# Kernel optimization log

Hardware: AMD Instinct MI355X
Metric: run time of the kernel (lower is better)

Reference implementation:

```python
import jax, jax.numpy as jnp
import numpy as np

N = 1 << 20          # number of segment duration values
NUM_EDGES = 100      # quantile bin edges (arange(0,1,0.01))
VOCAB = 101          # embedding rows
DIM = 128


def setup_inputs() -> dict:
    key = jax.random.key(0)
    k1, k2, k3 = jax.random.split(key, 3)
    # duration values in [0, 60) seconds
    time_value = jax.random.uniform(k1, (N,), dtype=jnp.float32) * 60.0
    # quantile edges of the duration distribution: sorted by construction
    bin_edges = jnp.sort(jax.random.uniform(k2, (NUM_EDGES,), dtype=jnp.float32) * 60.0)
    embed_table = jax.random.normal(k3, (VOCAB, DIM), dtype=jnp.float32)
    return {"time_value": time_value, "bin_edges": bin_edges, "embed_table": embed_table}


def reference(time_value, bin_edges, embed_table):
    # Fused, batched version of the original per-element loop:
    # torch.searchsorted(edges, dv) -> bucket index in [0, NUM_EDGES]
    idx = jnp.searchsorted(bin_edges, time_value, side="left")  # [N] int32
    # embedding lookup -> [N, DIM]
    return jnp.take(embed_table, idx, axis=0)
```

## Files before the change

kernel.cpp:

```cpp
#include <hip/hip_runtime.h>


#define MAX_EDGES 128
#define PAD_INF 3.402823466e+38f

__global__ __launch_bounds__(256) void compute_idx_kernel(
    const float* __restrict__ time_value,
    const float* __restrict__ bin_edges,
    int* __restrict__ idx,
    unsigned int n, int num_edges)
{
    __shared__ float s_edges[MAX_EDGES];
    if (threadIdx.x < MAX_EDGES)
        s_edges[threadIdx.x] = (threadIdx.x < (unsigned)num_edges)
                                   ? bin_edges[threadIdx.x] : PAD_INF;
    __syncthreads();

    const unsigned int stride = gridDim.x * blockDim.x;
    for (unsigned int i = blockIdx.x * blockDim.x + threadIdx.x;
         i < n; i += stride) {
        float v = time_value[i];
        int lo = 0;
        #pragma unroll
        for (int step = 64; step > 0; step >>= 1)
            lo += (s_edges[lo + step - 1] < v) ? step : 0;
        idx[i] = lo;
    }
}

__global__ __launch_bounds__(256) void gather_f4_32(
    const int* __restrict__ idx,
    const float* __restrict__ embed_table,
    float* __restrict__ out,
    unsigned int n)
{
    const float4* t4 = (const float4*)embed_table;
    float4* o4 = (float4*)out;

    const unsigned int total  = n << 3;
    const unsigned int stride = gridDim.x * blockDim.x;

    for (unsigned int j = blockIdx.x * blockDim.x + threadIdx.x;
         j < total; j += stride) {
        unsigned int row = j >> 3;
        unsigned int o   = j & 7u;
        unsigned int lo  = (unsigned int)idx[row];
        unsigned int tb  = (lo  << 5) + o;
        unsigned int ob  = (row << 5) + o;
        float4 a = t4[tb];
        float4 b = t4[tb + 8];
        float4 c = t4[tb + 16];
        float4 d = t4[tb + 24];
        o4[ob]      = a;
        o4[ob + 8]  = b;
        o4[ob + 16] = c;
        o4[ob + 24] = d;
    }
}

__device__ __forceinline__ int lower_bound_lds(const float* s_edges, int num_edges, float v) {
    int lo = 0, hi = num_edges;
    while (lo < hi) {
        int mid = (lo + hi) >> 1;
        if (s_edges[mid] < v) lo = mid + 1; else hi = mid;
    }
    return lo;
}

__global__ __launch_bounds__(256) void duration_encoding_generic(
    const float* __restrict__ time_value,
    const float* __restrict__ bin_edges,
    const float* __restrict__ embed_table,
    float* __restrict__ out,
    unsigned int n, int num_edges, unsigned int f4_per_row)
{
    __shared__ float s_edges[MAX_EDGES];
    for (int i = threadIdx.x; i < num_edges; i += blockDim.x)
        s_edges[i] = bin_edges[i];
    __syncthreads();

    const unsigned long long total  = (unsigned long long)n * f4_per_row;
    const unsigned long long stride = (unsigned long long)gridDim.x * blockDim.x;
    const float4* table4 = (const float4*)embed_table;
    float4* out4 = (float4*)out;

    for (unsigned long long j = (unsigned long long)blockIdx.x * blockDim.x + threadIdx.x;
         j < total; j += stride) {
        unsigned int row = (unsigned int)(j / f4_per_row);
        unsigned int c4  = (unsigned int)(j - (unsigned long long)row * f4_per_row);
        float v = time_value[row];
        int lo = lower_bound_lds(s_edges, num_edges, v);
        out4[j] = table4[(unsigned long long)lo * f4_per_row + c4];
    }
}

extern "C" void kernel_launch(void* const* d_in, const int* in_sizes, int n_in,
                              void* d_out, int out_size, void* d_ws, size_t ws_size,
                              hipStream_t stream) {
    const float* time_value  = (const float*)d_in[0];
    const float* bin_edges   = (const float*)d_in[1];
    const float* embed_table = (const float*)d_in[2];
    float* out = (float*)d_out;

    const unsigned int n         = (unsigned int)in_sizes[0];
    const int          num_edges = in_sizes[1];
    const unsigned int dim       = (unsigned int)(out_size / in_sizes[0]);
    const unsigned int f4_per_row = dim / 4;

    const int block = 256;

    if (f4_per_row == 32u && num_edges <= MAX_EDGES && ws_size >= (size_t)n * 4) {
        int* idx = (int*)d_ws;

        unsigned int b1 = (n + block - 1) / block;
        int grid1 = (int)(b1 < 4096u ? b1 : 4096u);
        compute_idx_kernel<<<grid1, block, 0, stream>>>(
            time_value, bin_edges, idx, n, num_edges);

        const unsigned int total = n << 3;
        unsigned int b2 = (total + block - 1) / block;
        int grid2 = (int)(b2 < 2048u ? b2 : 2048u);
        gather_f4_32<<<grid2, block, 0, stream>>>(idx, embed_table, out, n);
    } else {
        const unsigned long long total = (unsigned long long)n * f4_per_row;
        unsigned long long bn = (total + block - 1) / block;
        int grid = (int)(bn < 2048ull ? bn : 2048ull);
        duration_encoding_generic<<<grid, block, 0, stream>>>(
            time_value, bin_edges, embed_table, out, n, num_edges, f4_per_row);
    }
}
```

Measured before the change: 119.5 us.

## Vectorize index search and use one-shot strided gather without grid-stride loops

The index kernel now reads four time values per thread as a float4 and writes four indices as an int4, launching one thread per group of four with no grid-stride loop. The gather kernel drops its grid-stride loop and launches one thread per n*8 float4 slot. Each thread handles four float4s spaced T apart in the flattened output, so every store instruction across a wavefront is fully contiguous. The aim is to cut loop overhead and improve memory-level parallelism with larger grids. The trade-off is many more blocks and an extra idx load per float4.

After: 109.9 us. 8.0% less time.

```diff
diff --git a/kernel.cpp b/kernel.cpp
--- a/kernel.cpp
+++ b/kernel.cpp
@@ -4,7 +4,15 @@
 #define MAX_EDGES 128
 #define PAD_INF 3.402823466e+38f
 
-__global__ __launch_bounds__(256) void compute_idx_kernel(
+__device__ __forceinline__ int lb128(const float* s_edges, float v) {
+    int lo = 0;
+    #pragma unroll
+    for (int step = 64; step > 0; step >>= 1)
+        if (s_edges[lo + step - 1] < v) lo += step;
+    return lo;
+}
+
+__global__ __launch_bounds__(256) void compute_idx_vec4(
     const float* __restrict__ time_value,
     const float* __restrict__ bin_edges,
     int* __restrict__ idx,
@@ -16,46 +24,54 @@
                                    ? bin_edges[threadIdx.x] : PAD_INF;
     __syncthreads();
 
-    const unsigned int stride = gridDim.x * blockDim.x;
-    for (unsigned int i = blockIdx.x * blockDim.x + threadIdx.x;
-         i < n; i += stride) {
-        float v = time_value[i];
-        int lo = 0;
-        #pragma unroll
-        for (int step = 64; step > 0; step >>= 1)
-            lo += (s_edges[lo + step - 1] < v) ? step : 0;
-        idx[i] = lo;
+    const unsigned int nvec = n >> 2;
+    const unsigned int t = blockIdx.x * blockDim.x + threadIdx.x;
+    if (t < nvec) {
+        float4 v = ((const float4*)time_value)[t];
+        int4 r;
+        r.x = lb128(s_edges, v.x);
+        r.y = lb128(s_edges, v.y);
+        r.z = lb128(s_edges, v.z);
+        r.w = lb128(s_edges, v.w);
+        ((int4*)idx)[t] = r;
+    }
+    if (t == 0) {
+        for (unsigned int i = nvec << 2; i < n; ++i)
+            idx[i] = lb128(s_edges, time_value[i]);
     }
 }
 
-__global__ __launch_bounds__(256) void gather_f4_32(
+__global__ __launch_bounds__(256) void gather_strided4(
     const int* __restrict__ idx,
     const float* __restrict__ embed_table,
     float* __restrict__ out,
-    unsigned int n)
+    unsigned int T)
 {
     const float4* t4 = (const float4*)embed_table;
     float4* o4 = (float4*)out;
 
-    const unsigned int total  = n << 3;
-    const unsigned int stride = gridDim.x * blockDim.x;
+    const unsigned int t = blockIdx.x * blockDim.x + threadIdx.x;
+    if (t >= T) return;
 
-    for (unsigned int j = blockIdx.x * blockDim.x + threadIdx.x;
-         j < total; j += stride) {
-        unsigned int row = j >> 3;
-        unsigned int o   = j & 7u;
-        unsigned int lo  = (unsigned int)idx[row];
-        unsigned int tb  = (lo  << 5) + o;
-        unsigned int ob  = (row << 5) + o;
-        float4 a = t4[tb];
-        float4 b = t4[tb + 8];
-        float4 c = t4[tb + 16];
-        float4 d = t4[tb + 24];
-        o4[ob]      = a;
-        o4[ob + 8]  = b;
-        o4[ob + 16] = c;
-        o4[ob + 24] = d;
-    }
+    const unsigned int j0 = t;
+    const unsigned int j1 = t + T;
+    const unsigned int j2 = t + 2u * T;
+    const unsigned int j3 = t + 3u * T;
+
+    unsigned int r0 = (unsigned int)idx[j0 >> 5];
+    unsigned int r1 = (unsigned int)idx[j1 >> 5];
+    unsigned int r2 = (unsigned int)idx[j2 >> 5];
+    unsigned int r3 = (unsigned int)idx[j3 >> 5];
+
+    float4 a = t4[(r0 << 5) + (j0 & 31u)];
+    float4 b = t4[(r1 << 5) + (j1 & 31u)];
+    float4 c = t4[(r2 << 5) + (j2 & 31u)];
+    float4 d = t4[(r3 << 5) + (j3 & 31u)];
+
+    o4[j0] = a;
+    o4[j1] = b;
+    o4[j2] = c;
+    o4[j3] = d;
 }
 
 __device__ __forceinline__ int lower_bound_lds(const float* s_edges, int num_edges, float v) {
@@ -112,15 +128,15 @@
     if (f4_per_row == 32u && num_edges <= MAX_EDGES && ws_size >= (size_t)n * 4) {
         int* idx = (int*)d_ws;
 
-        unsigned int b1 = (n + block - 1) / block;
-        int grid1 = (int)(b1 < 4096u ? b1 : 4096u);
-        compute_idx_kernel<<<grid1, block, 0, stream>>>(
+        const unsigned int nvec = n >> 2;
+        unsigned int b1 = (nvec + block - 1) / block;
+        if (b1 == 0) b1 = 1;
+        compute_idx_vec4<<<(int)b1, block, 0, stream>>>(
             time_value, bin_edges, idx, n, num_edges);
 
-        const unsigned int total = n << 3;
-        unsigned int b2 = (total + block - 1) / block;
-        int grid2 = (int)(b2 < 2048u ? b2 : 2048u);
-        gather_f4_32<<<grid2, block, 0, stream>>>(idx, embed_table, out, n);
+        const unsigned int T = n << 3;
+        unsigned int b2 = (T + block - 1) / block;
+        gather_strided4<<<(int)b2, block, 0, stream>>>(idx, embed_table, out, T);
     } else {
         const unsigned long long total = (unsigned long long)n * f4_per_row;
         unsigned long long bn = (total + block - 1) / block;
```
